# Kernel optimization log

Measured on AMD Instinct MI355X. Metric: run time of the kernel, lower is better.

Reference implementation:

```python
import jax, jax.numpy as jnp
import numpy as np

N_NODES = 10000
N_EDGES = 160000
H = 128          # n_hidden_feat
K1 = 64          # n_Gaussian
K2 = 64          # n_grid_K**3
NB = 3           # N_block
G = 100          # number of graphs in batch
CUTOFF = 8.0


def setup_inputs() -> dict:
    key = jax.random.key(0)
    ks = jax.random.split(key, 20)
    s = 0.05
    return {
        'x': jax.random.normal(ks[0], (N_NODES, H), jnp.float32),
        'edge_distance': jax.random.uniform(ks[1], (N_EDGES,), jnp.float32, 0.5, 10.0),
        'combine_sets': jax.random.normal(ks[2], (N_EDGES, K1), jnp.float32),
        'plane_wave': jax.random.normal(ks[3], (N_EDGES, K2), jnp.float32),
        'emb_W': jax.random.normal(ks[4], (H, H), jnp.float32) * s,
        'conv_Wgate': jax.random.normal(ks[5], (NB, 3 * H, H), jnp.float32) * s,
        'conv_Wmlp': jax.random.normal(ks[6], (NB, 3 * H, H), jnp.float32) * s,
        'conv_W1': jax.random.normal(ks[7], (NB, K1, H), jnp.float32) * s,
        'conv_W2g': jax.random.normal(ks[8], (NB, K2, K2), jnp.float32) * s,
        'conv_W2': jax.random.normal(ks[9], (NB, K2, H), jnp.float32) * s,
        'pool_W1': jax.random.normal(ks[10], (NB, H, H), jnp.float32) * s,
        'pool_W2': jax.random.normal(ks[11], (NB, H, H), jnp.float32) * s,
        'psi_W': jax.random.normal(ks[12], (NB, H, H), jnp.float32) * s,
        'lr_W1': jax.random.normal(ks[13], (H, H // 2), jnp.float32) * s,
        'lr_W2': jax.random.normal(ks[14], (H // 2, H // 4), jnp.float32) * s,
        'edge_sources': jax.random.randint(ks[15], (N_EDGES,), 0, N_NODES, jnp.int32),
        'edge_targets': jax.random.randint(ks[16], (N_EDGES,), 0, N_NODES, jnp.int32),
        'graph_indices': jnp.sort(jax.random.randint(ks[17], (N_NODES,), 0, G, jnp.int32)),
        'node_counts': jax.random.randint(ks[18], (G,), 1, 200, jnp.int32),
    }


def reference(x, edge_distance, combine_sets, plane_wave, emb_W,
              conv_Wgate, conv_Wmlp, conv_W1, conv_W2g, conv_W2,
              pool_W1, pool_W2, psi_W, lr_W1, lr_W2,
              edge_sources, edge_targets, graph_indices, node_counts):
    n_graphs = node_counts.shape[0]
    elu = jax.nn.elu
    sig = jax.nn.sigmoid

    # NodeEmbedding (sigmoid activation, no bias)
    h = sig(x @ emb_W)                                   # [N, H]

    r = edge_distance[:, None]                           # [E, 1]
    mask = (r < CUTOFF).astype(h.dtype)                  # [E, 1]

    pooled_sum = jnp.zeros((n_graphs, h.shape[1]), h.dtype)
    for i in range(conv_Wgate.shape[0]):                 # N_block (small fixed)
        # --- GatedGraphConvolution ---
        ni = h[edge_sources]                             # [E, H] gather
        nj = h[edge_targets]                             # [E, H] gather
        fe = jnp.concatenate([ni, nj, (ni - nj) / r], axis=1)  # [E, 3H]
        e_gate = sig(fe @ conv_Wgate[i])                 # [E, H]
        e_mlp = elu(fe @ conv_Wmlp[i])                   # [E, H]
        z1 = combine_sets @ conv_W1[i]                   # [E, H]
        pw_gate = sig(plane_wave @ conv_W2g[i])          # [E, K2]
        z2 = (plane_wave * pw_gate) @ conv_W2[i]         # [E, H]
        z = e_gate * e_mlp * (z1 + z2) * mask            # [E, H]
        h = h.at[edge_sources].add(z)                    # scatter-add (index_add_)
        # --- Gated_pooling (note: original discards /node_counts -> sum pool) ---
        zp = elu((h @ pool_W1[i]) * (h @ pool_W2[i]))    # [N, H]
        pooled_sum = pooled_sum + jax.ops.segment_sum(zp, graph_indices, num_segments=n_graphs)
        # --- MLP_psi2n ---
        h = elu(h @ psi_W[i])

    y = elu(pooled_sum @ lr_W1)                          # [G, H/2]
    y = elu(y @ lr_W2)                                   # [G, H/4]
    return y
```

## Files before the change

kernel.cpp:

```cpp
#include <hip/hip_runtime.h>
#include <math.h>

#define H 128
#define N_NODES 10000
#define N_EDGES 160000

typedef float f32x4 __attribute__((ext_vector_type(4)));
typedef short s16x8 __attribute__((ext_vector_type(8)));

__device__ __forceinline__ float sigf(float x){ return 1.0f/(1.0f + __expf(-x)); }
__device__ __forceinline__ float eluf(float x){ return x > 0.0f ? x : (__expf(x) - 1.0f); }

__device__ __forceinline__ unsigned short f2bf(float f){
  unsigned int u = __float_as_uint(f);
  unsigned int r = (u + 0x7fffu + ((u >> 16) & 1u)) >> 16;
  return (unsigned short)r;
}
__device__ __forceinline__ float bf2f(unsigned short s){
  return __uint_as_float(((unsigned int)s) << 16);
}

__device__ __forceinline__ f32x4 MFMA16(s16x8 a, s16x8 b, f32x4 c){
  return __builtin_amdgcn_mfma_f32_16x16x32_bf16(a, b, c, 0, 0, 0);
}

__device__ __forceinline__ s16x8 loadA_f32(const float* p){
  float4 a = *(const float4*)p;
  float4 b = *(const float4*)(p+4);
  s16x8 r;
  r[0]=(short)f2bf(a.x); r[1]=(short)f2bf(a.y); r[2]=(short)f2bf(a.z); r[3]=(short)f2bf(a.w);
  r[4]=(short)f2bf(b.x); r[5]=(short)f2bf(b.y); r[6]=(short)f2bf(b.z); r[7]=(short)f2bf(b.w);
  return r;
}

__global__ __launch_bounds__(256) void hist_kernel(
    const int* __restrict__ src, const float* __restrict__ ed, int* __restrict__ count)
{
  int e = blockIdx.x*256 + threadIdx.x;
  if (e < N_EDGES && ed[e] < 8.0f) atomicAdd(&count[src[e]], 1);
}

__global__ __launch_bounds__(256) void scan_kernel(
    const int* __restrict__ count, int* __restrict__ offsets)
{
  __shared__ int tmp[256];
  __shared__ int sbase;
  if (threadIdx.x == 0) sbase = 0;
  __syncthreads();
  for (int c0 = 0; c0 < N_NODES; c0 += 256) {
    int i = c0 + threadIdx.x;
    int v = (i < N_NODES) ? count[i] : 0;
    tmp[threadIdx.x] = v;
    __syncthreads();
    for (int off = 1; off < 256; off <<= 1) {
      int t = (threadIdx.x >= off) ? tmp[threadIdx.x - off] : 0;
      __syncthreads();
      tmp[threadIdx.x] += t;
      __syncthreads();
    }
    if (i < N_NODES) offsets[i] = sbase + tmp[threadIdx.x] - v;
    __syncthreads();
    if (threadIdx.x == 255) sbase += tmp[255];
    __syncthreads();
  }
  if (threadIdx.x == 0) offsets[N_NODES] = sbase;
}

__global__ __launch_bounds__(256) void scatter_kernel(
    const int* __restrict__ src, const int* __restrict__ tgt, const float* __restrict__ ed,
    const int* __restrict__ offsets,
    int* __restrict__ cursor, int* __restrict__ mcur, int* __restrict__ perm,
    int* __restrict__ srcp, int* __restrict__ tgtp, float* __restrict__ edp)
{
  int e = blockIdx.x*256 + threadIdx.x;
  if (e < N_EDGES) {
    int s = src[e];
    float r = ed[e];
    int pos;
    if (r < 8.0f) pos = atomicAdd(&cursor[s], 1);
    else          pos = offsets[N_NODES] + atomicAdd(mcur, 1);
    perm[pos] = e;
    srcp[pos] = s;
    tgtp[pos] = tgt[e];
    edp[pos]  = r;
  }
}

__global__ __launch_bounds__(256) void prep_edges(
    const float* __restrict__ cs, const float* __restrict__ pw, const int* __restrict__ perm,
    unsigned short* __restrict__ csb, unsigned short* __restrict__ pwb)
{
  int idx = blockIdx.x*256 + threadIdx.x;
  if (idx >= N_EDGES*8) return;
  int pos = idx >> 3, kc = idx & 7;
  int e = perm[pos];
  s16x8 c = loadA_f32(&cs[(size_t)e*64 + kc*8]);
  s16x8 p = loadA_f32(&pw[(size_t)e*64 + kc*8]);
  *(s16x8*)&csb[(size_t)pos*64 + kc*8] = c;
  *(s16x8*)&pwb[(size_t)pos*64 + kc*8] = p;
}

__global__ __launch_bounds__(256) void prep_weights(
    const float* __restrict__ W1, const float* __restrict__ W2, const float* __restrict__ W2g,
    const float* __restrict__ embW,
    unsigned short* __restrict__ w1t, unsigned short* __restrict__ w2t,
    unsigned short* __restrict__ w2gt, unsigned short* __restrict__ embt)
{
  int idx = blockIdx.x*256 + threadIdx.x;
  if (idx < 3*8192) {
    int l = idx / 8192, r = idx % 8192;
    int c = r >> 6, k = r & 63;
    w1t[idx] = f2bf(W1[l*8192 + k*128 + c]);
    w2t[idx] = f2bf(W2[l*8192 + k*128 + c]);
  } else if (idx < 3*8192 + 3*4096) {
    int idx2 = idx - 3*8192;
    int l = idx2 / 4096, r = idx2 % 4096;
    int c = r >> 6, k = r & 63;
    w2gt[idx2] = f2bf(W2g[l*4096 + k*64 + c]);
  } else {
    int idx3 = idx - (3*8192 + 3*4096);
    if (idx3 < 16384) {
      int c = idx3 >> 7, k = idx3 & 127;
      embt[idx3] = f2bf(embW[k*128 + c]);
    }
  }
}

__global__ __launch_bounds__(256) void prep_nodew(
    const float* __restrict__ Wg, const float* __restrict__ Wm,
    const float* __restrict__ p1, const float* __restrict__ p2, const float* __restrict__ psiW,
    unsigned short* __restrict__ wnt, unsigned short* __restrict__ wpt)
{
  int idx = blockIdx.x*256 + threadIdx.x;
  if (idx < 3*98304) {
    int l = idx / 98304, r = idx % 98304;
    int j = r >> 7, k = r & 127;
    float v;
    if (j < 384) v = Wg[l*49152 + (j>>7)*16384 + k*128 + (j&127)];
    else { int jj = j - 384; v = Wm[l*49152 + (jj>>7)*16384 + k*128 + (jj&127)]; }
    wnt[idx] = f2bf(v);
  } else {
    int idx2 = idx - 3*98304;
    if (idx2 < 3*49152) {
      int l = idx2 / 49152, r = idx2 % 49152;
      int j = r >> 7, k = r & 127;
      float v;
      if (j < 128)      v = p1 [l*16384 + k*128 + j];
      else if (j < 256) v = p2 [l*16384 + k*128 + (j-128)];
      else              v = psiW[l*16384 + k*128 + (j-256)];
      wpt[idx2] = f2bf(v);
    }
  }
}

__global__ __launch_bounds__(256) void embed_mfma(
    const float* __restrict__ x, const unsigned short* __restrict__ embt,
    float* __restrict__ h_out)
{
  int tid = threadIdx.x, wave = tid >> 6, lane = tid & 63;
  int row = lane & 15, kg = lane >> 4;
  int nbase = blockIdx.x*32 + (wave & 1)*16;
  int hf = (wave >> 1) * 64;
  int nA = nbase + row;
  int nclamp = nA < N_NODES ? nA : N_NODES-1;
  const float* xr = &x[(size_t)nclamp*H];
  s16x8 a[4];
  #pragma unroll
  for (int ks = 0; ks < 4; ks++) a[ks] = loadA_f32(xr + ks*32 + kg*8);

  f32x4 acc[4];
  #pragma unroll
  for (int t = 0; t < 4; t++) { acc[t][0]=0.f; acc[t][1]=0.f; acc[t][2]=0.f; acc[t][3]=0.f; }
  #pragma unroll
  for (int t = 0; t < 4; t++) {
    int col = hf + t*16 + row;
    #pragma unroll
    for (int ks = 0; ks < 4; ks++) {
      s16x8 b = *(const s16x8*)&embt[(size_t)col*128 + ks*32 + kg*8];
      acc[t] = MFMA16(a[ks], b, acc[t]);
    }
  }
  #pragma unroll
  for (int r = 0; r < 4; r++) {
    int nc = nbase + kg*4 + r;
    if (nc >= N_NODES) continue;
    #pragma unroll
    for (int t = 0; t < 4; t++) {
      int col = hf + t*16 + row;
      h_out[(size_t)nc*H + col] = sigf(acc[t][r]);
    }
  }
}

__global__ __launch_bounds__(256) void nodeA_mfma(
    const float* __restrict__ h, const unsigned short* __restrict__ wnt,
    unsigned short* __restrict__ spackb, unsigned short* __restrict__ tpackb)
{
  int tid = threadIdx.x, wave = tid >> 6, lane = tid & 63;
  int row = lane & 15, kg = lane >> 4;
  int nbase = blockIdx.x*32 + (wave & 1)*16;
  int tw = (wave >> 1) * 4;
  int nA = nbase + row;
  int nclamp = nA < N_NODES ? nA : N_NODES-1;
  const float* hr = &h[(size_t)nclamp*H];
  s16x8 a[4];
  #pragma unroll
  for (int ks = 0; ks < 4; ks++) a[ks] = loadA_f32(hr + ks*32 + kg*8);

  #pragma unroll
  for (int ti = 0; ti < 4; ti++) {
    int t = tw + ti;
    f32x4 acc[6];
    #pragma unroll
    for (int ch = 0; ch < 6; ch++) { acc[ch][0]=0.f; acc[ch][1]=0.f; acc[ch][2]=0.f; acc[ch][3]=0.f; }
    #pragma unroll
    for (int ch = 0; ch < 6; ch++) {
      int col = ch*128 + t*16 + row;
      #pragma unroll
      for (int ks = 0; ks < 4; ks++) {
        s16x8 b = *(const s16x8*)&wnt[(size_t)col*128 + ks*32 + kg*8];
        acc[ch] = MFMA16(a[ks], b, acc[ch]);
      }
    }
    int c = t*16 + row;
    #pragma unroll
    for (int r = 0; r < 4; r++) {
      int nc = nbase + kg*4 + r;
      if (nc >= N_NODES) continue;
      size_t base = (size_t)nc*512 + c*4;
      unsigned int s0 = (unsigned int)f2bf(acc[0][r]) | ((unsigned int)f2bf(acc[2][r]) << 16);
      unsigned int s1 = (unsigned int)f2bf(acc[3][r]) | ((unsigned int)f2bf(acc[5][r]) << 16);
      unsigned int t0 = (unsigned int)f2bf(acc[1][r]) | ((unsigned int)f2bf(acc[2][r]) << 16);
      unsigned int t1 = (unsigned int)f2bf(acc[4][r]) | ((unsigned int)f2bf(acc[5][r]) << 16);
      *(uint2*)&spackb[base] = make_uint2(s0, s1);
      *(uint2*)&tpackb[base] = make_uint2(t0, t1);
    }
  }
}

__global__ __launch_bounds__(256) void fused_edge(
    float* __restrict__ h_acc,
    const unsigned short* __restrict__ csb, const unsigned short* __restrict__ pwb,
    const unsigned short* __restrict__ w1t, const unsigned short* __restrict__ w2t,
    const unsigned short* __restrict__ w2gt,
    const int* __restrict__ srcp, const int* __restrict__ tgtp,
    const float* __restrict__ edp, const int* __restrict__ nact,
    const unsigned short* __restrict__ spackb, const unsigned short* __restrict__ tpackb)
{
  __shared__ unsigned short gate[64*64];
  __shared__ unsigned short zb[64][132];
  __shared__ int   src_s[64];
  __shared__ int   tgt_s[64];
  __shared__ float rcp_s[64];
  __shared__ float msk_s[64];

  int p0 = blockIdx.x * 64;
  if (p0 >= *nact) return;

  int tid  = threadIdx.x;
  int wave = tid >> 6, lane = tid & 63;
  int row  = lane & 15, kg = lane >> 4;

  if (tid < 64) {
    float r = edp[p0 + tid];
    rcp_s[tid] = 1.0f / r;
    msk_s[tid] = (r < 8.0f) ? 1.0f : 0.0f;
    src_s[tid] = srcp[p0 + tid];
    tgt_s[tid] = tgtp[p0 + tid];
  }

  int pos = p0 + wave*16 + row;
  s16x8 acs[2], apw[2];
  acs[0] = *(const s16x8*)&csb[(size_t)pos*64 + kg*8];
  acs[1] = *(const s16x8*)&csb[(size_t)pos*64 + 32 + kg*8];
  apw[0] = *(const s16x8*)&pwb[(size_t)pos*64 + kg*8];
  apw[1] = *(const s16x8*)&pwb[(size_t)pos*64 + 32 + kg*8];

  f32x4 acc1[4];
  #pragma unroll
  for (int nt = 0; nt < 4; nt++) { acc1[nt][0]=0.f; acc1[nt][1]=0.f; acc1[nt][2]=0.f; acc1[nt][3]=0.f; }
  #pragma unroll
  for (int nt = 0; nt < 4; nt++) {
    s16x8 b0 = *(const s16x8*)&w2gt[(size_t)(nt*16+row)*64 + kg*8];
    s16x8 b1 = *(const s16x8*)&w2gt[(size_t)(nt*16+row)*64 + 32 + kg*8];
    acc1[nt] = MFMA16(apw[0], b0, acc1[nt]);
    acc1[nt] = MFMA16(apw[1], b1, acc1[nt]);
  }

  #pragma unroll
  for (int nt = 0; nt < 4; nt++) {
    #pragma unroll
    for (int r = 0; r < 4; r++) {
      int grow = wave*16 + kg*4 + r;
      int gcol = nt*16 + row;
      int byt = (grow << 7) + (gcol << 1);
      byt ^= (grow & 7) << 4;
      *(unsigned short*)((char*)gate + byt) = f2bf(sigf(acc1[nt][r]));
    }
  }
  __syncthreads();

  s16x8 apg[2];
  #pragma unroll
  for (int ks = 0; ks < 2; ks++) {
    int arow = wave*16 + row;
    int byt = (arow << 7) + ks*64 + kg*16;
    byt ^= (arow & 7) << 4;
    s16x8 g = *(s16x8*)((char*)gate + byt);
    s16x8 o;
    #pragma unroll
    for (int j = 0; j < 8; j++) {
      float v = bf2f((unsigned short)apw[ks][j]) * bf2f((unsigned short)g[j]);
      o[j] = (short)f2bf(v);
    }
    apg[ks] = o;
  }

  f32x4 acc2[8];
  #pragma unroll
  for (int nt = 0; nt < 8; nt++) { acc2[nt][0]=0.f; acc2[nt][1]=0.f; acc2[nt][2]=0.f; acc2[nt][3]=0.f; }
  #pragma unroll
  for (int nt = 0; nt < 8; nt++) {
    #pragma unroll
    for (int ks = 0; ks < 2; ks++) {
      s16x8 b1 = *(const s16x8*)&w1t[(size_t)(nt*16+row)*64 + ks*32 + kg*8];
      acc2[nt] = MFMA16(acs[ks], b1, acc2[nt]);
      s16x8 b2 = *(const s16x8*)&w2t[(size_t)(nt*16+row)*64 + ks*32 + kg*8];
      acc2[nt] = MFMA16(apg[ks], b2, acc2[nt]);
    }
  }

  #pragma unroll
  for (int nt = 0; nt < 8; nt++) {
    #pragma unroll
    for (int r = 0; r < 4; r++) {
      zb[wave*16 + kg*4 + r][nt*16 + row] = f2bf(acc2[nt][r]);
    }
  }
  __syncthreads();

  {
    int l = lane;
    int e0 = wave*16;
    int cur = src_s[e0];
    s16x8 sp = *(const s16x8*)&spackb[(size_t)cur*512 + l*8];
    float Ags0 = bf2f((unsigned short)sp[0]), Cgs0 = bf2f((unsigned short)sp[1]);
    float Ams0 = bf2f((unsigned short)sp[2]), Cms0 = bf2f((unsigned short)sp[3]);
    float Ags1 = bf2f((unsigned short)sp[4]), Cgs1 = bf2f((unsigned short)sp[5]);
    float Ams1 = bf2f((unsigned short)sp[6]), Cms1 = bf2f((unsigned short)sp[7]);
    float acc0 = 0.f, accB = 0.f;
    for (int eb = e0; eb < e0 + 16; eb += 4) {
      s16x8 tp[4]; unsigned int zz[4];
      #pragma unroll
      for (int b = 0; b < 4; b++) {
        int e = eb + b;
        tp[b] = *(const s16x8*)&tpackb[(size_t)tgt_s[e]*512 + l*8];
        zz[b] = *(const unsigned int*)&zb[e][2*l];
      }
      #pragma unroll
      for (int b = 0; b < 4; b++) {
        int e = eb + b;
        int sn = src_s[e];
        if (sn != cur) {
          atomicAdd(&h_acc[(size_t)cur*H + 2*l],     acc0);
          atomicAdd(&h_acc[(size_t)cur*H + 2*l + 1], accB);
          acc0 = 0.f; accB = 0.f; cur = sn;
          sp = *(const s16x8*)&spackb[(size_t)cur*512 + l*8];
          Ags0 = bf2f((unsigned short)sp[0]); Cgs0 = bf2f((unsigned short)sp[1]);
          Ams0 = bf2f((unsigned short)sp[2]); Cms0 = bf2f((unsigned short)sp[3]);
          Ags1 = bf2f((unsigned short)sp[4]); Cgs1 = bf2f((unsigned short)sp[5]);
          Ams1 = bf2f((unsigned short)sp[6]); Cms1 = bf2f((unsigned short)sp[7]);
        }
        float rc = rcp_s[e], mk = msk_s[e];
        float z0 = bf2f((unsigned short)(zz[b] & 0xffffu));
        float z1 = bf2f((unsigned short)(zz[b] >> 16));
        float Bg0 = bf2f((unsigned short)tp[b][0]), Cg0 = bf2f((unsigned short)tp[b][1]);
        float Bm0 = bf2f((unsigned short)tp[b][2]), Cm0 = bf2f((unsigned short)tp[b][3]);
        float Bg1 = bf2f((unsigned short)tp[b][4]), Cg1 = bf2f((unsigned short)tp[b][5]);
        float Bm1 = bf2f((unsigned short)tp[b][6]), Cm1 = bf2f((unsigned short)tp[b][7]);
        float g0 = sigf(Ags0 + Bg0 + rc*(Cgs0 - Cg0));
        float m0 = eluf(Ams0 + Bm0 + rc*(Cms0 - Cm0));
        acc0 += g0 * m0 * z0 * mk;
        float g1 = sigf(Ags1 + Bg1 + rc*(Cgs1 - Cg1));
        float m1 = eluf(Ams1 + Bm1 + rc*(Cms1 - Cm1));
        accB += g1 * m1 * z1 * mk;
      }
    }
    atomicAdd(&h_acc[(size_t)cur*H + 2*l],     acc0);
    atomicAdd(&h_acc[(size_t)cur*H + 2*l + 1], accB);
  }
}

__global__ __launch_bounds__(256) void node_next(
    float* __restrict__ h,
    const unsigned short* __restrict__ wpt,
    const unsigned short* __restrict__ wnt,
    const int* __restrict__ gidx, float* __restrict__ pooled,
    unsigned short* __restrict__ spackb, unsigned short* __restrict__ tpackb,
    int has_next)
{
  __shared__ unsigned short hb[32*128];
  int tid = threadIdx.x, wave = tid >> 6, lane = tid & 63;
  int row = lane & 15, kg = lane >> 4;
  int nh = wave & 1, hf = (wave >> 1)*64;
  int nbase = blockIdx.x*32 + nh*16;
  int nA = nbase + row;
  int nclamp = nA < N_NODES ? nA : N_NODES-1;
  const float* hr = &h[(size_t)nclamp*H];
  s16x8 a[4];
  #pragma unroll
  for (int ks = 0; ks < 4; ks++) a[ks] = loadA_f32(hr + ks*32 + kg*8);

  f32x4 acc1[4], acc2[4], acc3[4];
  #pragma unroll
  for (int t = 0; t < 4; t++) {
    #pragma unroll
    for (int r = 0; r < 4; r++) { acc1[t][r]=0.f; acc2[t][r]=0.f; acc3[t][r]=0.f; }
  }
  #pragma unroll
  for (int t = 0; t < 4; t++) {
    int col = hf + t*16 + row;
    #pragma unroll
    for (int ks = 0; ks < 4; ks++) {
      s16x8 b1 = *(const s16x8*)&wpt[(size_t)(col      )*128 + ks*32 + kg*8];
      s16x8 b2 = *(const s16x8*)&wpt[(size_t)(col + 128)*128 + ks*32 + kg*8];
      s16x8 b3 = *(const s16x8*)&wpt[(size_t)(col + 256)*128 + ks*32 + kg*8];
      acc1[t] = MFMA16(a[ks], b1, acc1[t]);
      acc2[t] = MFMA16(a[ks], b2, acc2[t]);
      acc3[t] = MFMA16(a[ks], b3, acc3[t]);
    }
  }

  int nc0 = nbase + kg*4;
  int g0 = (nc0     < N_NODES) ? gidx[nc0]     : -1;
  int g3 = (nc0 + 3 < N_NODES) ? gidx[nc0 + 3] : -2;
  if (g0 == g3) {
    #pragma unroll
    for (int t = 0; t < 4; t++) {
      int col = hf + t*16 + row;
      float s = 0.f;
      #pragma unroll
      for (int r = 0; r < 4; r++) s += eluf(acc1[t][r] * acc2[t][r]);
      atomicAdd(&pooled[g0*H + col], s);
      #pragma unroll
      for (int r = 0; r < 4; r++) {
        float v = eluf(acc3[t][r]);
        h[(size_t)(nc0 + r)*H + col] = v;
        int ln = nh*16 + kg*4 + r;
        int byt = (ln << 8) + (col << 1);
        byt ^= (ln & 7) << 4;
        *(unsigned short*)((char*)hb + byt) = f2bf(v);
      }
    }
  } else {
    #pragma unroll
    for (int r = 0; r < 4; r++) {
      int nc = nc0 + r;
      int ln = nh*16 + kg*4 + r;
      bool ok = nc < N_NODES;
      int g = ok ? gidx[nc] : 0;
      #pragma unroll
      for (int t = 0; t < 4; t++) {
        int col = hf + t*16 + row;
        float zp = ok ? eluf(acc1[t][r] * acc2[t][r]) : 0.f;
        if (ok) atomicAdd(&pooled[g*H + col], zp);
        float v = eluf(acc3[t][r]);
        if (ok) h[(size_t)nc*H + col] = v;
        int byt = (ln << 8) + (col << 1);
        byt ^= (ln & 7) << 4;
        *(unsigned short*)((char*)hb + byt) = f2bf(v);
      }
    }
  }
  if (!has_next) return;
  __syncthreads();

  int rt = wave & 1;
  int tw = (wave >> 1) * 4;
  int arow = rt*16 + row;
  s16x8 an[4];
  #pragma unroll
  for (int ks = 0; ks < 4; ks++) {
    int byt = (arow << 8) + ks*64 + kg*16;
    byt ^= (arow & 7) << 4;
    an[ks] = *(s16x8*)((char*)hb + byt);
  }
  int nb2 = blockIdx.x*32 + rt*16;
  #pragma unroll
  for (int ti = 0; ti < 4; ti++) {
    int t = tw + ti;
    f32x4 acc[6];
    #pragma unroll
    for (int ch = 0; ch < 6; ch++) { acc[ch][0]=0.f; acc[ch][1]=0.f; acc[ch][2]=0.f; acc[ch][3]=0.f; }
    #pragma unroll
    for (int ch = 0; ch < 6; ch++) {
      int col = ch*128 + t*16 + row;
      #pragma unroll
      for (int ks = 0; ks < 4; ks++) {
        s16x8 b = *(const s16x8*)&wnt[(size_t)col*128 + ks*32 + kg*8];
        acc[ch] = MFMA16(an[ks], b, acc[ch]);
      }
    }
    int c = t*16 + row;
    #pragma unroll
    for (int r = 0; r < 4; r++) {
      int nc = nb2 + kg*4 + r;
      if (nc >= N_NODES) continue;
      size_t base = (size_t)nc*512 + c*4;
      unsigned int s0 = (unsigned int)f2bf(acc[0][r]) | ((unsigned int)f2bf(acc[2][r]) << 16);
      unsigned int s1 = (unsigned int)f2bf(acc[3][r]) | ((unsigned int)f2bf(acc[5][r]) << 16);
      unsigned int t0 = (unsigned int)f2bf(acc[1][r]) | ((unsigned int)f2bf(acc[2][r]) << 16);
      unsigned int t1 = (unsigned int)f2bf(acc[4][r]) | ((unsigned int)f2bf(acc[5][r]) << 16);
      *(uint2*)&spackb[base] = make_uint2(s0, s1);
      *(uint2*)&tpackb[base] = make_uint2(t0, t1);
    }
  }
}

__global__ __launch_bounds__(64) void final_kernel(
    const float* __restrict__ pooled, const float* __restrict__ lr1, const float* __restrict__ lr2,
    float* __restrict__ out)
{
  __shared__ float sp[128];
  __shared__ float y1[64];
  int g = blockIdx.x, tid = threadIdx.x;
  sp[tid]      = pooled[g*128 + tid];
  sp[tid + 64] = pooled[g*128 + 64 + tid];
  __syncthreads();
  float acc = 0.f;
  for (int k = 0; k < 128; k++) acc += sp[k] * lr1[k*64 + tid];
  y1[tid] = eluf(acc);
  __syncthreads();
  if (tid < 32) {
    float a2 = 0.f;
    for (int k = 0; k < 64; k++) a2 += y1[k] * lr2[k*32 + tid];
    out[g*32 + tid] = eluf(a2);
  }
}

extern "C" void kernel_launch(void* const* d_in, const int* in_sizes, int n_in,
                              void* d_out, int out_size, void* d_ws, size_t ws_size,
                              hipStream_t stream)
{
  const float* x    = (const float*)d_in[0];
  const float* ed   = (const float*)d_in[1];
  const float* cs   = (const float*)d_in[2];
  const float* pw   = (const float*)d_in[3];
  const float* embW = (const float*)d_in[4];
  const float* Wg   = (const float*)d_in[5];
  const float* Wm   = (const float*)d_in[6];
  const float* W1   = (const float*)d_in[7];
  const float* W2g  = (const float*)d_in[8];
  const float* W2   = (const float*)d_in[9];
  const float* p1   = (const float*)d_in[10];
  const float* p2   = (const float*)d_in[11];
  const float* psiW = (const float*)d_in[12];
  const float* lr1  = (const float*)d_in[13];
  const float* lr2  = (const float*)d_in[14];
  const int* esrc   = (const int*)d_in[15];
  const int* etgt   = (const int*)d_in[16];
  const int* gidx   = (const int*)d_in[17];

  float* h_b    = (float*)d_ws;
  float* pooled = h_b + (size_t)N_NODES*H;
  unsigned short* spackb = (unsigned short*)(pooled + 100*H);
  unsigned short* tpackb = spackb + (size_t)N_NODES*512;
  int* counts  = (int*)(tpackb + (size_t)N_NODES*512);
  int* offsets = counts + N_NODES;
  int* cursor  = offsets + N_NODES + 1;
  int* mcur    = cursor + N_NODES;
  int* perm    = mcur + 1;
  int* srcp    = perm + N_EDGES;
  int* tgtp    = srcp + N_EDGES;
  float* edp   = (float*)(tgtp + N_EDGES);
  unsigned short* w1t  = (unsigned short*)(edp + N_EDGES);
  unsigned short* w2t  = w1t + 3*8192;
  unsigned short* w2gt = w2t + 3*8192;
  unsigned short* embt = w2gt + 3*4096;
  unsigned short* wnt  = embt + 16384;
  unsigned short* wpt  = wnt + 3*98304;
  unsigned short* csb  = wpt + 3*49152;
  unsigned short* pwb  = csb + (size_t)N_EDGES*64;

  hipMemsetAsync(counts, 0, N_NODES*sizeof(int), stream);
  hipMemsetAsync(mcur, 0, sizeof(int), stream);
  hipMemsetAsync(pooled, 0, 100*H*sizeof(float), stream);
  hist_kernel<<<(N_EDGES+255)/256, 256, 0, stream>>>(esrc, ed, counts);
  scan_kernel<<<1, 256, 0, stream>>>(counts, offsets);
  hipMemcpyAsync(cursor, offsets, N_NODES*sizeof(int), hipMemcpyDeviceToDevice, stream);
  scatter_kernel<<<(N_EDGES+255)/256, 256, 0, stream>>>(esrc, etgt, ed, offsets,
      cursor, mcur, perm, srcp, tgtp, edp);
  prep_edges<<<N_EDGES*8/256, 256, 0, stream>>>(cs, pw, perm, csb, pwb);
  prep_weights<<<208, 256, 0, stream>>>(W1, W2, W2g, embW, w1t, w2t, w2gt, embt);
  prep_nodew<<<(3*98304 + 3*49152 + 255)/256, 256, 0, stream>>>(Wg, Wm, p1, p2, psiW, wnt, wpt);

  embed_mfma<<<(N_NODES+31)/32, 256, 0, stream>>>(x, embt, h_b);
  nodeA_mfma<<<(N_NODES+31)/32, 256, 0, stream>>>(h_b, wnt, spackb, tpackb);

  for (int i = 0; i < 3; i++) {
    fused_edge<<<N_EDGES/64, 256, 0, stream>>>(h_b, csb, pwb,
        w1t + i*8192, w2t + i*8192, w2gt + i*4096,
        srcp, tgtp, edp, offsets + N_NODES, spackb, tpackb);
    node_next<<<(N_NODES+31)/32, 256, 0, stream>>>(h_b,
        wpt + i*49152, wnt + ((i+1) % 3)*98304,
        gidx, pooled, spackb, tpackb, (i < 2) ? 1 : 0);
  }
  final_kernel<<<100, 64, 0, stream>>>(pooled, lr1, lr2, (float*)d_out);
}
```

Baseline: 458.6 us.

## Fuse embedding with first node projection and halve node tile per block

```diff
diff --git a/kernel.cpp b/kernel.cpp
--- a/kernel.cpp
+++ b/kernel.cpp
@@ -153,85 +153,79 @@
   }
 }
 
-__global__ __launch_bounds__(256) void embed_mfma(
+__global__ __launch_bounds__(256) void embed_pack(
     const float* __restrict__ x, const unsigned short* __restrict__ embt,
-    float* __restrict__ h_out)
-{
+    const unsigned short* __restrict__ wnt,
+    float* __restrict__ h_out,
+    unsigned short* __restrict__ spackb, unsigned short* __restrict__ tpackb)
+{
+  __shared__ unsigned short hb[16*128];
   int tid = threadIdx.x, wave = tid >> 6, lane = tid & 63;
   int row = lane & 15, kg = lane >> 4;
-  int nbase = blockIdx.x*32 + (wave & 1)*16;
-  int hf = (wave >> 1) * 64;
-  int nA = nbase + row;
-  int nclamp = nA < N_NODES ? nA : N_NODES-1;
-  const float* xr = &x[(size_t)nclamp*H];
+  int nbase = blockIdx.x*16;
+  const float* xr = &x[(size_t)(nbase + row)*H];
   s16x8 a[4];
   #pragma unroll
   for (int ks = 0; ks < 4; ks++) a[ks] = loadA_f32(xr + ks*32 + kg*8);
 
-  f32x4 acc[4];
-  #pragma unroll
-  for (int t = 0; t < 4; t++) { acc[t][0]=0.f; acc[t][1]=0.f; acc[t][2]=0.f; acc[t][3]=0.f; }
-  #pragma unroll
-  for (int t = 0; t < 4; t++) {
-    int col = hf + t*16 + row;
+  f32x4 acc[2];
+  #pragma unroll
+  for (int ti = 0; ti < 2; ti++) { acc[ti][0]=0.f; acc[ti][1]=0.f; acc[ti][2]=0.f; acc[ti][3]=0.f; }
+  #pragma unroll
+  for (int ti = 0; ti < 2; ti++) {
+    int col = (wave*2 + ti)*16 + row;
     #pragma unroll
     for (int ks = 0; ks < 4; ks++) {
       s16x8 b = *(const s16x8*)&embt[(size_t)col*128 + ks*32 + kg*8];
-      acc[t] = MFMA16(a[ks], b, acc[t]);
-    }
-  }
-  #pragma unroll
-  for (int r = 0; r < 4; r++) {
-    int nc = nbase + kg*4 + r;
-    if (nc >= N_NODES) continue;
-    #pragma unroll
-    for (int t = 0; t < 4; t++) {
-      int col = hf + t*16 + row;
-      h_out[(size_t)nc*H + col] = sigf(acc[t][r]);
-    }
-  }
-}
-
-__global__ __launch_bounds__(256) void nodeA_mfma(
-    const float* __restrict__ h, const unsigned short* __restrict__ wnt,
-    unsigned short* __restrict__ spackb, unsigned short* __restrict__ tpackb)
-{
-  int tid = threadIdx.x, wave = tid >> 6, lane = tid & 63;
-  int row = lane & 15, kg = lane >> 4;
-  int nbase = blockIdx.x*32 + (wave & 1)*16;
-  int tw = (wave >> 1) * 4;
-  int nA = nbase + row;
-  int nclamp = nA < N_NODES ? nA : N_NODES-1;
-  const float* hr = &h[(size_t)nclamp*H];
-  s16x8 a[4];
-  #pragma unroll
-  for (int ks = 0; ks < 4; ks++) a[ks] = loadA_f32(hr + ks*32 + kg*8);
-
-  #pragma unroll
-  for (int ti = 0; ti < 4; ti++) {
-    int t = tw + ti;
-    f32x4 acc[6];
-    #pragma unroll
-    for (int ch = 0; ch < 6; ch++) { acc[ch][0]=0.f; acc[ch][1]=0.f; acc[ch][2]=0.f; acc[ch][3]=0.f; }
+      acc[ti] = MFMA16(a[ks], b, acc[ti]);
+    }
+  }
+  #pragma unroll
+  for (int ti = 0; ti < 2; ti++) {
+    int col = (wave*2 + ti)*16 + row;
+    #pragma unroll
+    for (int r = 0; r < 4; r++) {
+      int ln = kg*4 + r;
+      float v = sigf(acc[ti][r]);
+      h_out[(size_t)(nbase + ln)*H + col] = v;
+      int byt = (ln << 8) + (col << 1);
+      byt ^= (ln & 7) << 4;
+      *(unsigned short*)((char*)hb + byt) = f2bf(v);
+    }
+  }
+  __syncthreads();
+
+  s16x8 an[4];
+  #pragma unroll
+  for (int ks = 0; ks < 4; ks++) {
+    int byt = (row << 8) + ks*64 + kg*16;
+    byt ^= (row & 7) << 4;
+    an[ks] = *(s16x8*)((char*)hb + byt);
+  }
+  #pragma unroll
+  for (int ti = 0; ti < 2; ti++) {
+    int t = wave*2 + ti;
+    f32x4 pacc[6];
+    #pragma unroll
+    for (int ch = 0; ch < 6; ch++) { pacc[ch][0]=0.f; pacc[ch][1]=0.f; pacc[ch][2]=0.f; pacc[ch][3]=0.f; }
     #pragma unroll
     for (int ch = 0; ch < 6; ch++) {
       int col = ch*128 + t*16 + row;
       #pragma unroll
       for (int ks = 0; ks < 4; ks++) {
         s16x8 b = *(const s16x8*)&wnt[(size_t)col*128 + ks*32 + kg*8];
-        acc[ch] = MFMA16(a[ks], b, acc[ch]);
+        pacc[ch] = MFMA16(an[ks], b, pacc[ch]);
       }
     }
     int c = t*16 + row;
     #pragma unroll
     for (int r = 0; r < 4; r++) {
       int nc = nbase + kg*4 + r;
-      if (nc >= N_NODES) continue;
       size_t base = (size_t)nc*512 + c*4;
-      unsigned int s0 = (unsigned int)f2bf(acc[0][r]) | ((unsigned int)f2bf(acc[2][r]) << 16);
-      unsigned int s1 = (unsigned int)f2bf(acc[3][r]) | ((unsigned int)f2bf(acc[5][r]) << 16);
-      unsigned int t0 = (unsigned int)f2bf(acc[1][r]) | ((unsigned int)f2bf(acc[2][r]) << 16);
-      unsigned int t1 = (unsigned int)f2bf(acc[4][r]) | ((unsigned int)f2bf(acc[5][r]) << 16);
+      unsigned int s0 = (unsigned int)f2bf(pacc[0][r]) | ((unsigned int)f2bf(pacc[2][r]) << 16);
+      unsigned int s1 = (unsigned int)f2bf(pacc[3][r]) | ((unsigned int)f2bf(pacc[5][r]) << 16);
+      unsigned int t0 = (unsigned int)f2bf(pacc[1][r]) | ((unsigned int)f2bf(pacc[2][r]) << 16);
+      unsigned int t1 = (unsigned int)f2bf(pacc[4][r]) | ((unsigned int)f2bf(pacc[5][r]) << 16);
       *(uint2*)&spackb[base] = make_uint2(s0, s1);
       *(uint2*)&tpackb[base] = make_uint2(t0, t1);
     }
@@ -247,12 +241,12 @@
     const float* __restrict__ edp, const int* __restrict__ nact,
     const unsigned short* __restrict__ spackb, const unsigned short* __restrict__ tpackb)
 {
-  __shared__ unsigned short gate[64*64];
   __shared__ unsigned short zb[64][132];
   __shared__ int   src_s[64];
   __shared__ int   tgt_s[64];
   __shared__ float rcp_s[64];
   __shared__ float msk_s[64];
+  unsigned short* gate = &zb[0][0];
 
   int p0 = blockIdx.x * 64;
   if (p0 >= *nact) return;
@@ -315,6 +309,7 @@
     }
     apg[ks] = o;
   }
+  __syncthreads();
 
   f32x4 acc2[8];
   #pragma unroll
@@ -399,54 +394,50 @@
     unsigned short* __restrict__ spackb, unsigned short* __restrict__ tpackb,
     int has_next)
 {
-  __shared__ unsigned short hb[32*128];
+  __shared__ unsigned short hb[16*128];
   int tid = threadIdx.x, wave = tid >> 6, lane = tid & 63;
   int row = lane & 15, kg = lane >> 4;
-  int nh = wave & 1, hf = (wave >> 1)*64;
-  int nbase = blockIdx.x*32 + nh*16;
-  int nA = nbase + row;
-  int nclamp = nA < N_NODES ? nA : N_NODES-1;
-  const float* hr = &h[(size_t)nclamp*H];
+  int nbase = blockIdx.x*16;
+  const float* hr = &h[(size_t)(nbase + row)*H];
   s16x8 a[4];
   #pragma unroll
   for (int ks = 0; ks < 4; ks++) a[ks] = loadA_f32(hr + ks*32 + kg*8);
 
-  f32x4 acc1[4], acc2[4], acc3[4];
-  #pragma unroll
-  for (int t = 0; t < 4; t++) {
-    #pragma unroll
-    for (int r = 0; r < 4; r++) { acc1[t][r]=0.f; acc2[t][r]=0.f; acc3[t][r]=0.f; }
-  }
-  #pragma unroll
-  for (int t = 0; t < 4; t++) {
-    int col = hf + t*16 + row;
+  f32x4 acc1[2], acc2[2], acc3[2];
+  #pragma unroll
+  for (int ti = 0; ti < 2; ti++) {
+    #pragma unroll
+    for (int r = 0; r < 4; r++) { acc1[ti][r]=0.f; acc2[ti][r]=0.f; acc3[ti][r]=0.f; }
+  }
+  #pragma unroll
+  for (int ti = 0; ti < 2; ti++) {
+    int col = (wave*2 + ti)*16 + row;
     #pragma unroll
     for (int ks = 0; ks < 4; ks++) {
       s16x8 b1 = *(const s16x8*)&wpt[(size_t)(col      )*128 + ks*32 + kg*8];
       s16x8 b2 = *(const s16x8*)&wpt[(size_t)(col + 128)*128 + ks*32 + kg*8];
       s16x8 b3 = *(const s16x8*)&wpt[(size_t)(col + 256)*128 + ks*32 + kg*8];
-      acc1[t] = MFMA16(a[ks], b1, acc1[t]);
-      acc2[t] = MFMA16(a[ks], b2, acc2[t]);
-      acc3[t] = MFMA16(a[ks], b3, acc3[t]);
+      acc1[ti] = MFMA16(a[ks], b1, acc1[ti]);
+      acc2[ti] = MFMA16(a[ks], b2, acc2[ti]);
+      acc3[ti] = MFMA16(a[ks], b3, acc3[ti]);
     }
   }
 
   int nc0 = nbase + kg*4;
-  int g0 = (nc0     < N_NODES) ? gidx[nc0]     : -1;
-  int g3 = (nc0 + 3 < N_NODES) ? gidx[nc0 + 3] : -2;
+  int g0 = gidx[nc0], g3 = gidx[nc0 + 3];
   if (g0 == g3) {
     #pragma unroll
-    for (int t = 0; t < 4; t++) {
-      int col = hf + t*16 + row;
+    for (int ti = 0; ti < 2; ti++) {
+      int col = (wave*2 + ti)*16 + row;
       float s = 0.f;
       #pragma unroll
-      for (int r = 0; r < 4; r++) s += eluf(acc1[t][r] * acc2[t][r]);
+      for (int r = 0; r < 4; r++) s += eluf(acc1[ti][r] * acc2[ti][r]);
       atomicAdd(&pooled[g0*H + col], s);
       #pragma unroll
       for (int r = 0; r < 4; r++) {
-        float v = eluf(acc3[t][r]);
+        int ln = kg*4 + r;
+        float v = eluf(acc3[ti][r]);
         h[(size_t)(nc0 + r)*H + col] = v;
-        int ln = nh*16 + kg*4 + r;
         int byt = (ln << 8) + (col << 1);
         byt ^= (ln & 7) << 4;
         *(unsigned short*)((char*)hb + byt) = f2bf(v);
@@ -456,16 +447,15 @@
     #pragma unroll
     for (int r = 0; r < 4; r++) {
       int nc = nc0 + r;
-      int ln = nh*16 + kg*4 + r;
-      bool ok = nc < N_NODES;
-      int g = ok ? gidx[nc] : 0;
-      #pragma unroll
-      for (int t = 0; t < 4; t++) {
-        int col = hf + t*16 + row;
-        float zp = ok ? eluf(acc1[t][r] * acc2[t][r]) : 0.f;
-        if (ok) atomicAdd(&pooled[g*H + col], zp);
-        float v = eluf(acc3[t][r]);
-        if (ok) h[(size_t)nc*H + col] = v;
+      int ln = kg*4 + r;
+      int g = gidx[nc];
+      #pragma unroll
+      for (int ti = 0; ti < 2; ti++) {
+        int col = (wave*2 + ti)*16 + row;
+        float zp = eluf(acc1[ti][r] * acc2[ti][r]);
+        atomicAdd(&pooled[g*H + col], zp);
+        float v = eluf(acc3[ti][r]);
+        h[(size_t)nc*H + col] = v;
         int byt = (ln << 8) + (col << 1);
         byt ^= (ln & 7) << 4;
         *(unsigned short*)((char*)hb + byt) = f2bf(v);
@@ -475,42 +465,37 @@
   if (!has_next) return;
   __syncthreads();
 
-  int rt = wave & 1;
-  int tw = (wave >> 1) * 4;
-  int arow = rt*16 + row;
   s16x8 an[4];
   #pragma unroll
   for (int ks = 0; ks < 4; ks++) {
-    int byt = (arow << 8) + ks*64 + kg*16;
-    byt ^= (arow & 7) << 4;
+    int byt = (row << 8) + ks*64 + kg*16;
+    byt ^= (row & 7) << 4;
     an[ks] = *(s16x8*)((char*)hb + byt);
   }
-  int nb2 = blockIdx.x*32 + rt*16;
-  #pragma unroll
-  for (int ti = 0; ti < 4; ti++) {
-    int t = tw + ti;
-    f32x4 acc[6];
-    #pragma unroll
-    for (int ch = 0; ch < 6; ch++) { acc[ch][0]=0.f; acc[ch][1]=0.f; acc[ch][2]=0.f; acc[ch][3]=0.f; }
+  #pragma unroll
+  for (int ti = 0; ti < 2; ti++) {
+    int t = wave*2 + ti;
+    f32x4 pacc[6];
+    #pragma unroll
+    for (int ch = 0; ch < 6; ch++) { pacc[ch][0]=0.f; pacc[ch][1]=0.f; pacc[ch][2]=0.f; pacc[ch][3]=0.f; }
     #pragma unroll
     for (int ch = 0; ch < 6; ch++) {
       int col = ch*128 + t*16 + row;
       #pragma unroll
       for (int ks = 0; ks < 4; ks++) {
         s16x8 b = *(const s16x8*)&wnt[(size_t)col*128 + ks*32 + kg*8];
-        acc[ch] = MFMA16(an[ks], b, acc[ch]);
+        pacc[ch] = MFMA16(an[ks], b, pacc[ch]);
       }
     }
     int c = t*16 + row;
     #pragma unroll
     for (int r = 0; r < 4; r++) {
-      int nc = nb2 + kg*4 + r;
-      if (nc >= N_NODES) continue;
+      int nc = nbase + kg*4 + r;
       size_t base = (size_t)nc*512 + c*4;
-      unsigned int s0 = (unsigned int)f2bf(acc[0][r]) | ((unsigned int)f2bf(acc[2][r]) << 16);
-      unsigned int s1 = (unsigned int)f2bf(acc[3][r]) | ((unsigned int)f2bf(acc[5][r]) << 16);
-      unsigned int t0 = (unsigned int)f2bf(acc[1][r]) | ((unsigned int)f2bf(acc[2][r]) << 16);
-      unsigned int t1 = (unsigned int)f2bf(acc[4][r]) | ((unsigned int)f2bf(acc[5][r]) << 16);
+      unsigned int s0 = (unsigned int)f2bf(pacc[0][r]) | ((unsigned int)f2bf(pacc[2][r]) << 16);
+      unsigned int s1 = (unsigned int)f2bf(pacc[3][r]) | ((unsigned int)f2bf(pacc[5][r]) << 16);
+      unsigned int t0 = (unsigned int)f2bf(pacc[1][r]) | ((unsigned int)f2bf(pacc[2][r]) << 16);
+      unsigned int t1 = (unsigned int)f2bf(pacc[4][r]) | ((unsigned int)f2bf(pacc[5][r]) << 16);
       *(uint2*)&spackb[base] = make_uint2(s0, s1);
       *(uint2*)&tpackb[base] = make_uint2(t0, t1);
     }
@@ -594,14 +579,13 @@
   prep_weights<<<208, 256, 0, stream>>>(W1, W2, W2g, embW, w1t, w2t, w2gt, embt);
   prep_nodew<<<(3*98304 + 3*49152 + 255)/256, 256, 0, stream>>>(Wg, Wm, p1, p2, psiW, wnt, wpt);
 
-  embed_mfma<<<(N_NODES+31)/32, 256, 0, stream>>>(x, embt, h_b);
-  nodeA_mfma<<<(N_NODES+31)/32, 256, 0, stream>>>(h_b, wnt, spackb, tpackb);
+  embed_pack<<<N_NODES/16, 256, 0, stream>>>(x, embt, wnt, h_b, spackb, tpackb);
 
   for (int i = 0; i < 3; i++) {
     fused_edge<<<N_EDGES/64, 256, 0, stream>>>(h_b, csb, pwb,
         w1t + i*8192, w2t + i*8192, w2gt + i*4096,
         srcp, tgtp, edp, offsets + N_NODES, spackb, tpackb);
-    node_next<<<(N_NODES+31)/32, 256, 0, stream>>>(h_b,
+    node_next<<<N_NODES/16, 256, 0, stream>>>(h_b,
         wpt + i*49152, wnt + ((i+1) % 3)*98304,
         gidx, pooled, spackb, tpackb, (i < 2) ? 1 : 0);
   }
```

Result: faster. 428.4 us (-6.6%).
